# Kernel optimization log

Hardware: AMD Instinct MI355X
Metric: run time of the kernel (lower is better)

## Reference

```python
import jax, jax.numpy as jnp
import numpy as np

N_NODES = 50000
N_EDGES = 800000
HID = 128
EDGE_DIM = 4
LAYERS = 4
MAX_Z = 100
NUM_GRAPHS = 512


def setup_inputs() -> dict:
    key = jax.random.key(0)
    ks = jax.random.split(key, 16)
    s = lambda k, shape, fan_in: jax.random.normal(k, shape, jnp.float32) / np.sqrt(fan_in)
    inp = {
        "z": jax.random.randint(ks[0], (N_NODES,), 0, MAX_Z + 1),
        "edge_index": jax.random.randint(ks[1], (2, N_EDGES), 0, N_NODES),
        "edge_attr": jax.random.normal(ks[2], (N_EDGES, EDGE_DIM), jnp.float32),
        "batch": jnp.sort(jax.random.randint(ks[3], (N_NODES,), 0, NUM_GRAPHS)),
        "emb": jax.random.normal(ks[4], (MAX_Z + 1, HID), jnp.float32),
        # stacked per-layer params; Linear stored as [in, out]
        "ew1": s(ks[5], (LAYERS, 2 * HID + EDGE_DIM, HID), 2 * HID + EDGE_DIM),
        "eb1": jnp.zeros((LAYERS, HID), jnp.float32),
        "ew2": s(ks[6], (LAYERS, HID, HID), HID),
        "eb2": jnp.zeros((LAYERS, HID), jnp.float32),
        "nw": s(ks[7], (LAYERS, 2 * HID, HID), 2 * HID),
        "nb": jnp.zeros((LAYERS, HID), jnp.float32),
        "rw1": s(ks[8], (HID, HID), HID),
        "rb1": jnp.zeros((HID,), jnp.float32),
        "rw2": s(ks[9], (HID, 1), HID),
        "rb2": jnp.zeros((1,), jnp.float32),
    }
    return inp


def _forward(z, edge_index, edge_attr, batch,
             emb, ew1, eb1, ew2, eb2, nw, nb, rw1, rb1, rw2, rb2):
    silu = jax.nn.silu
    src, dst = edge_index[0], edge_index[1]
    x = emb[z]  # [N, H]
    for l in range(LAYERS):
        m_in = jnp.concatenate([x[src], x[dst], edge_attr], axis=-1)  # [E, 2H+ed]
        h = silu(m_in @ ew1[l] + eb1[l])
        msg = silu(h @ ew2[l] + eb2[l])  # [E, H]
        agg = jax.ops.segment_sum(msg, dst, num_segments=N_NODES)  # scatter-add
        x = silu(jnp.concatenate([x, agg], axis=-1) @ nw[l] + nb[l])
    # segment mean over graphs
    sums = jax.ops.segment_sum(x, batch, num_segments=NUM_GRAPHS)
    counts = jnp.clip(jax.ops.segment_sum(jnp.ones((x.shape[0],), x.dtype), batch,
                                          num_segments=NUM_GRAPHS), 1.0)[:, None]
    g = sums / counts  # [G, H]
    pred = (silu(g @ rw1 + rb1) @ rw2 + rb2)[:, 0]  # [G]
    return pred


def reference(z, edge_index, edge_attr, batch,
              emb, ew1, eb1, ew2, eb2, nw, nb, rw1, rb1, rw2, rb2):
    return _forward(z, edge_index, edge_attr, batch,
                    emb, ew1, eb1, ew2, eb2, nw, nb, rw1, rb1, rw2, rb2)
```

## Files before the change

kernel.cpp:

```cpp
#include <hip/hip_runtime.h>
#include <math.h>

#define HID  128
#define EDIM 4

typedef unsigned short u16;
typedef u16    us8   __attribute__((ext_vector_type(8)));
typedef __bf16 bf16x8 __attribute__((ext_vector_type(8)));
typedef float  f32x4 __attribute__((ext_vector_type(4)));

__device__ __forceinline__ float silu_f(float v) {
    return v * __builtin_amdgcn_rcpf(1.0f + __expf(-v));
}
__device__ __forceinline__ u16 f2bf(float f) {
    unsigned u = __float_as_uint(f);
    unsigned r = u + 0x7fffu + ((u >> 16) & 1u);
    return (u16)(r >> 16);
}
__device__ __forceinline__ u16 f2bf_fast(float f) {
    return (u16)((__float_as_uint(f) + 0x8000u) >> 16);
}
__device__ __forceinline__ unsigned pack_bf2(float a, float b) {
    return ((__float_as_uint(a) + 0x8000u) >> 16) |
           ((__float_as_uint(b) + 0x8000u) & 0xffff0000u);
}
__device__ __forceinline__ float bf2f(u16 s) {
    return __uint_as_float(((unsigned)s) << 16);
}
__device__ __forceinline__ bf16x8 as_bf(us8 v) {
    return __builtin_bit_cast(bf16x8, v);
}

__device__ __forceinline__ void wfrag_gen(const float* __restrict__ w,
        u16* __restrict__ out, int KT, int Kdata, int Kstride,
        int split, int jump, int idx) {
    int lane = idx & 63;
    int f    = (idx >> 6) % (KT * 8);
    int l    = idx / (64 * KT * 8);
    int kt = f >> 3, nt = f & 7;
    int n  = nt * 16 + (lane & 15);
    int k0 = kt * 32 + ((lane >> 4) * 8);
    us8 v;
    #pragma unroll
    for (int j = 0; j < 8; ++j) {
        int k = k0 + j;
        int row = k + (k >= split ? jump : 0);
        v[j] = (row < Kdata) ? f2bf(w[((size_t)l * Kstride + row) * HID + n]) : (u16)0;
    }
    *(us8*)&out[((size_t)(l * KT * 8 + f) * 64 + lane) * 8] = v;
}

#define T1S (4 * 4 * 8 * 64)
#define T1T (4 * 1 * 8 * 64)
#define T1B (4 * 4 * 8 * 64)
#define T2  (4 * 4 * 8 * 64)
#define T3  (4 * 8 * 8 * 64)

__global__ __launch_bounds__(256) void setup_kernel(
        const float* __restrict__ ew1, const float* __restrict__ ew2,
        const float* __restrict__ nw,
        u16* __restrict__ w1sf, u16* __restrict__ w1tf,
        u16* __restrict__ w1bf,
        u16* __restrict__ w2f, u16* __restrict__ nwf,
        int* __restrict__ cnt, int* __restrict__ cursor,
        float* __restrict__ sums, float* __restrict__ cnts_g, int N, int G) {
    const int BIG = 1 << 30;
    int idx = blockIdx.x * 256 + threadIdx.x;
    if (idx < T1S) { wfrag_gen(ew1, w1sf, 4, 128, 260, BIG, 0, idx); return; }
    idx -= T1S;
    if (idx < T1T) { wfrag_gen(ew1, w1tf, 1, 260, 260, 0, 256, idx); return; }
    idx -= T1T;
    if (idx < T1B) { wfrag_gen(ew1, w1bf, 4, 260, 260, 0, 128, idx); return; }
    idx -= T1B;
    if (idx < T2) { wfrag_gen(ew2, w2f, 4, 128, 128, BIG, 0, idx); return; }
    idx -= T2;
    if (idx < T3) { wfrag_gen(nw, nwf, 8, 256, 256, BIG, 0, idx); return; }
    idx -= T3;
    if (idx < N) { cnt[idx] = 0; return; }
    idx -= N;
    if (idx < N) { cursor[idx] = 0; return; }
    idx -= N;
    if (idx < G * HID) { sums[idx] = 0.f; return; }
    idx -= G * HID;
    if (idx < G) { cnts_g[idx] = 0.f; return; }
}

__global__ __launch_bounds__(256) void hist_kernel(const int* __restrict__ dst,
        int* __restrict__ cnt, int E) {
    int e = blockIdx.x * 256 + threadIdx.x;
    if (e < E) atomicAdd(&cnt[dst[e]], 1);
}

__global__ __launch_bounds__(1024) void scan_kernel(const int* __restrict__ cnt,
        int* __restrict__ rowptr, int n) {
    __shared__ int s[1024];
    const int t = threadIdx.x;
    const int chunk = (n + 1023) >> 10;
    int lo = t * chunk, hi = lo + chunk;
    if (lo > n) lo = n;
    if (hi > n) hi = n;
    int sum = 0;
    for (int i = lo; i < hi; ++i) sum += cnt[i];
    s[t] = sum;
    __syncthreads();
    for (int off = 1; off < 1024; off <<= 1) {
        int v = (t >= off) ? s[t - off] : 0;
        __syncthreads();
        s[t] += v;
        __syncthreads();
    }
    int run = s[t] - sum;
    for (int i = lo; i < hi; ++i) { rowptr[i] = run; run += cnt[i]; }
    if (t == 1023) rowptr[n] = run;
}

__global__ __launch_bounds__(256) void scatter_kernel(const int* __restrict__ src,
        const int* __restrict__ dst, const float* __restrict__ ea,
        const int* __restrict__ rowptr, int* __restrict__ cursor,
        int* __restrict__ srcS, int* __restrict__ dstS, u16* __restrict__ eaS, int E) {
    int e = blockIdx.x * 256 + threadIdx.x;
    if (e >= E) return;
    int d = dst[e];
    int p = rowptr[d] + atomicAdd(&cursor[d], 1);
    srcS[p] = src[e];
    dstS[p] = d;
    const float* q = &ea[(size_t)e * EDIM];
    ushort4 v;
    v.x = f2bf(q[0]); v.y = f2bf(q[1]); v.z = f2bf(q[2]); v.w = f2bf(q[3]);
    *(ushort4*)&eaS[(size_t)p * 4] = v;
}

__global__ __launch_bounds__(HID) void embed_kernel(const int* __restrict__ z,
        const float* __restrict__ emb, u16* __restrict__ xb,
        float* __restrict__ agg, const int* __restrict__ batch,
        float* __restrict__ counts, int n) {
    int i = blockIdx.x;
    if (i >= n) return;
    int t = threadIdx.x;
    xb[(size_t)i * HID + t] = f2bf(emb[(size_t)z[i] * HID + t]);
    agg[(size_t)i * HID + t] = 0.f;
    if (t == 0) unsafeAtomicAdd(&counts[batch[i]], 1.0f);
}

__global__ __launch_bounds__(256) void ys_kernel(
        const u16* __restrict__ xb, const u16* __restrict__ w1sf,
        const u16* __restrict__ w1bf,
        float* __restrict__ Ys, float* __restrict__ Y, int n) {
    const int t    = threadIdx.x;
    const int i0   = blockIdx.x * 32;
    const int wv   = t >> 6, lane = t & 63;
    const int lrow = lane & 15;
    const int kq   = lane >> 4;
    const int kq8  = kq * 8;

    int iN[2];
    #pragma unroll
    for (int mt = 0; mt < 2; ++mt) {
        int i = i0 + mt * 16 + lrow; if (i >= n) i = n - 1;
        iN[mt] = i;
    }
    f32x4 aS[2][2], aB[2][2];
    #pragma unroll
    for (int mt = 0; mt < 2; ++mt)
        #pragma unroll
        for (int nt = 0; nt < 2; ++nt) {
            aS[mt][nt] = (f32x4){0.f, 0.f, 0.f, 0.f};
            aB[mt][nt] = (f32x4){0.f, 0.f, 0.f, 0.f};
        }

    #pragma unroll
    for (int kt = 0; kt < 4; ++kt) {
        bf16x8 ws0 = *(const bf16x8*)&w1sf[((size_t)(kt * 8 + wv * 2 + 0) * 64 + lane) * 8];
        bf16x8 ws1 = *(const bf16x8*)&w1sf[((size_t)(kt * 8 + wv * 2 + 1) * 64 + lane) * 8];
        bf16x8 wb0 = *(const bf16x8*)&w1bf[((size_t)(kt * 8 + wv * 2 + 0) * 64 + lane) * 8];
        bf16x8 wb1 = *(const bf16x8*)&w1bf[((size_t)(kt * 8 + wv * 2 + 1) * 64 + lane) * 8];
        #pragma unroll
        for (int mt = 0; mt < 2; ++mt) {
            bf16x8 a = as_bf(*(const us8*)&xb[(size_t)iN[mt] * HID + kt * 32 + kq8]);
            aS[mt][0] = __builtin_amdgcn_mfma_f32_16x16x32_bf16(ws0, a, aS[mt][0], 0, 0, 0);
            aS[mt][1] = __builtin_amdgcn_mfma_f32_16x16x32_bf16(ws1, a, aS[mt][1], 0, 0, 0);
            aB[mt][0] = __builtin_amdgcn_mfma_f32_16x16x32_bf16(wb0, a, aB[mt][0], 0, 0, 0);
            aB[mt][1] = __builtin_amdgcn_mfma_f32_16x16x32_bf16(wb1, a, aB[mt][1], 0, 0, 0);
        }
    }
    #pragma unroll
    for (int mt = 0; mt < 2; ++mt) {
        int node = i0 + mt * 16 + lrow;
        if (node < n) {
            #pragma unroll
            for (int nt = 0; nt < 2; ++nt) {
                *(f32x4*)&Ys[(size_t)node * HID + (wv * 2 + nt) * 16 + kq * 4] = aS[mt][nt];
                *(f32x4*)&Y [(size_t)node * HID + (wv * 2 + nt) * 16 + kq * 4] = aB[mt][nt];
            }
        }
    }
}

__global__ __launch_bounds__(512, 8) void edge_mfma(
        const int* __restrict__ srcS, const int* __restrict__ dstS,
        const u16* __restrict__ eaS,
        const u16* __restrict__ w1tf, const float* __restrict__ b1,
        const u16* __restrict__ w2f, const float* __restrict__ b2,
        const float* __restrict__ Ys, const float* __restrict__ Y,
        float* __restrict__ agg, int nE) {
    __shared__ __align__(16) char smem[64 * 132 * 4];
    __shared__ __align__(16) int dsh[64];
    __shared__ __align__(16) int ssh[64];
    u16*   A = (u16*)smem;
    u16*   H = (u16*)smem;
    float* M = (float*)smem;

    const int t    = threadIdx.x;
    const int e0   = blockIdx.x * 64;
    const int wv   = t >> 6, lane = t & 63;
    const int lrow = lane & 15;
    const int kq   = lane >> 4;
    const int kq8  = kq * 8;
    const int rq   = kq * 4;
    const int h    = wv >> 2;
    const int p    = wv & 3;

    if (t < 64) {
        int e = e0 + t;
        bool valid = e < nE; if (!valid) e = nE - 1;
        dsh[t] = valid ? dstS[e] : -1;
        ssh[t] = srcS[e];
        ushort4 q = *(const ushort4*)&eaS[(size_t)e * 4];
        int base = t * 40;
        us8 z8 = (us8){0, 0, 0, 0, 0, 0, 0, 0};
        *(us8*)&A[base + 8]  = z8;
        *(us8*)&A[base + 16] = z8;
        *(us8*)&A[base + 24] = z8;
        A[base + 0] = q.x; A[base + 1] = q.y; A[base + 2] = q.z; A[base + 3] = q.w;
        A[base + 4] = 0;   A[base + 5] = 0;   A[base + 6] = 0;   A[base + 7] = 0;
    }
    __syncthreads();

    f32x4 acc[2][2];
    #pragma unroll
    for (int mt = 0; mt < 2; ++mt) {
        int edge = (h * 2 + mt) * 16 + lrow;
        int d = dsh[edge]; if (d < 0) d = 0;
        int s = ssh[edge];
        #pragma unroll
        for (int nt = 0; nt < 2; ++nt) {
            f32x4 bv = *(const f32x4*)&b1[(p * 2 + nt) * 16 + rq];
            f32x4 yv = *(const f32x4*)&Y [(size_t)d * HID + (p * 2 + nt) * 16 + rq];
            f32x4 sv = *(const f32x4*)&Ys[(size_t)s * HID + (p * 2 + nt) * 16 + rq];
            acc[mt][nt] = bv + yv + sv;
        }
    }
    {
        bf16x8 w0 = *(const bf16x8*)&w1tf[((size_t)(p * 2 + 0) * 64 + lane) * 8];
        bf16x8 w1 = *(const bf16x8*)&w1tf[((size_t)(p * 2 + 1) * 64 + lane) * 8];
        #pragma unroll
        for (int mt = 0; mt < 2; ++mt) {
            bf16x8 a = *(const bf16x8*)&A[((h * 2 + mt) * 16 + lrow) * 40 + kq8];
            acc[mt][0] = __builtin_amdgcn_mfma_f32_16x16x32_bf16(w0, a, acc[mt][0], 0, 0, 0);
            acc[mt][1] = __builtin_amdgcn_mfma_f32_16x16x32_bf16(w1, a, acc[mt][1], 0, 0, 0);
        }
    }
    __syncthreads();

    #pragma unroll
    for (int mt = 0; mt < 2; ++mt)
        #pragma unroll
        for (int nt = 0; nt < 2; ++nt) {
            uint2 hv;
            hv.x = pack_bf2(silu_f(acc[mt][nt][0]), silu_f(acc[mt][nt][1]));
            hv.y = pack_bf2(silu_f(acc[mt][nt][2]), silu_f(acc[mt][nt][3]));
            int edge = (h * 2 + mt) * 16 + lrow;
            *(uint2*)&H[edge * 136 + (p * 2 + nt) * 16 + rq] = hv;
        }
    __syncthreads();

    f32x4 acc2[2][2];
    #pragma unroll
    for (int nt = 0; nt < 2; ++nt) {
        f32x4 bv = *(const f32x4*)&b2[(p * 2 + nt) * 16 + rq];
        acc2[0][nt] = bv; acc2[1][nt] = bv;
    }
    #pragma unroll
    for (int kt = 0; kt < 4; ++kt) {
        bf16x8 w0 = *(const bf16x8*)&w2f[((size_t)(kt * 8 + p * 2 + 0) * 64 + lane) * 8];
        bf16x8 w1 = *(const bf16x8*)&w2f[((size_t)(kt * 8 + p * 2 + 1) * 64 + lane) * 8];
        #pragma unroll
        for (int mt = 0; mt < 2; ++mt) {
            bf16x8 a = *(const bf16x8*)&H[((h * 2 + mt) * 16 + lrow) * 136 + kt * 32 + kq8];
            acc2[mt][0] = __builtin_amdgcn_mfma_f32_16x16x32_bf16(w0, a, acc2[mt][0], 0, 0, 0);
            acc2[mt][1] = __builtin_amdgcn_mfma_f32_16x16x32_bf16(w1, a, acc2[mt][1], 0, 0, 0);
        }
    }
    __syncthreads();

    #pragma unroll
    for (int mt = 0; mt < 2; ++mt)
        #pragma unroll
        for (int nt = 0; nt < 2; ++nt) {
            f32x4 mv;
            #pragma unroll
            for (int r = 0; r < 4; ++r) mv[r] = silu_f(acc2[mt][nt][r]);
            int edge = (h * 2 + mt) * 16 + lrow;
            *(f32x4*)&M[edge * 132 + (p * 2 + nt) * 16 + rq] = mv;
        }

    {
        int col = p * 32 + (lane & 31);
        int r0  = h * 32 + (lane >> 5) * 16;
        int4 da = *(const int4*)&dsh[r0];
        int4 db = *(const int4*)&dsh[r0 + 4];
        int4 dc = *(const int4*)&dsh[r0 + 8];
        int4 dd = *(const int4*)&dsh[r0 + 12];
        int ds_[16] = {da.x, da.y, da.z, da.w, db.x, db.y, db.z, db.w,
                       dc.x, dc.y, dc.z, dc.w, dd.x, dd.y, dd.z, dd.w};
        float run = 0.f;
        int   cur = ds_[0];
        #pragma unroll
        for (int i = 0; i < 16; ++i) {
            run += M[(r0 + i) * 132 + col];
            int nxt = (i == 15) ? -2 : ds_[i + 1];
            if (cur != nxt) {
                if (cur >= 0)
                    unsafeAtomicAdd(&agg[(size_t)cur * HID + col], run);
                run = 0.f; cur = nxt;
            }
        }
    }
}

__global__ __launch_bounds__(256) void node_mfma(
        u16* __restrict__ xb, float* __restrict__ agg,
        const u16* __restrict__ nwf, const float* __restrict__ nb,
        const int* __restrict__ batch, float* __restrict__ sums,
        int last, int n) {
    const int t    = threadIdx.x;
    const int i0   = blockIdx.x * 32;
    const int wv   = t >> 6, lane = t & 63;
    const int lrow = lane & 15;
    const int kq   = lane >> 4;
    const int kq8  = kq * 8;
    const int rq   = kq * 4;

    int iN[2];
    #pragma unroll
    for (int mt = 0; mt < 2; ++mt) {
        int i = i0 + mt * 16 + lrow; if (i >= n) i = n - 1;
        iN[mt] = i;
    }

    f32x4 acc[2][2];
    {
        float bias0 = nb[wv * 32 + lrow], bias1 = nb[wv * 32 + 16 + lrow];
        #pragma unroll
        for (int mt = 0; mt < 2; ++mt)
            #pragma unroll
            for (int r = 0; r < 4; ++r) {
                acc[mt][0][r] = bias0; acc[mt][1][r] = bias1;
            }
    }
    #pragma unroll
    for (int kt = 0; kt < 4; ++kt) {
        bf16x8 w0 = *(const bf16x8*)&nwf[((size_t)(kt * 8 + wv * 2 + 0) * 64 + lane) * 8];
        bf16x8 w1 = *(const bf16x8*)&nwf[((size_t)(kt * 8 + wv * 2 + 1) * 64 + lane) * 8];
        #pragma unroll
        for (int mt = 0; mt < 2; ++mt) {
            bf16x8 a = as_bf(*(const us8*)&xb[(size_t)iN[mt] * HID + kt * 32 + kq8]);
            acc[mt][0] = __builtin_amdgcn_mfma_f32_16x16x32_bf16(a, w0, acc[mt][0], 0, 0, 0);
            acc[mt][1] = __builtin_amdgcn_mfma_f32_16x16x32_bf16(a, w1, acc[mt][1], 0, 0, 0);
        }
    }
    #pragma unroll
    for (int kt = 4; kt < 8; ++kt) {
        bf16x8 w0 = *(const bf16x8*)&nwf[((size_t)(kt * 8 + wv * 2 + 0) * 64 + lane) * 8];
        bf16x8 w1 = *(const bf16x8*)&nwf[((size_t)(kt * 8 + wv * 2 + 1) * 64 + lane) * 8];
        #pragma unroll
        for (int mt = 0; mt < 2; ++mt) {
            const float* pa = &agg[(size_t)iN[mt] * HID + (kt - 4) * 32 + kq8];
            float4 f0 = *(const float4*)pa;
            float4 f1 = *(const float4*)(pa + 4);
            us8 av;
            av[0] = f2bf_fast(f0.x); av[1] = f2bf_fast(f0.y);
            av[2] = f2bf_fast(f0.z); av[3] = f2bf_fast(f0.w);
            av[4] = f2bf_fast(f1.x); av[5] = f2bf_fast(f1.y);
            av[6] = f2bf_fast(f1.z); av[7] = f2bf_fast(f1.w);
            bf16x8 a = as_bf(av);
            acc[mt][0] = __builtin_amdgcn_mfma_f32_16x16x32_bf16(a, w0, acc[mt][0], 0, 0, 0);
            acc[mt][1] = __builtin_amdgcn_mfma_f32_16x16x32_bf16(a, w1, acc[mt][1], 0, 0, 0);
        }
    }

    if (!last) {
        __syncthreads();
        const float4 z4 = make_float4(0.f, 0.f, 0.f, 0.f);
        #pragma unroll
        for (int kt = 0; kt < 4; ++kt)
            #pragma unroll
            for (int mt = 0; mt < 2; ++mt) {
                float* pa = &agg[(size_t)iN[mt] * HID + kt * 32 + kq8];
                *(float4*)pa = z4; *(float4*)(pa + 4) = z4;
            }
        #pragma unroll
        for (int mt = 0; mt < 2; ++mt)
            #pragma unroll
            for (int nt2 = 0; nt2 < 2; ++nt2)
                #pragma unroll
                for (int r = 0; r < 4; ++r) {
                    int i = i0 + mt * 16 + rq + r;
                    if (i < n)
                        xb[(size_t)i * HID + wv * 32 + nt2 * 16 + lrow] =
                            f2bf_fast(silu_f(acc[mt][nt2][r]));
                }
    } else {
        #pragma unroll
        for (int mt = 0; mt < 2; ++mt)
            #pragma unroll
            for (int nt2 = 0; nt2 < 2; ++nt2)
                #pragma unroll
                for (int r = 0; r < 4; ++r) {
                    int i = i0 + mt * 16 + rq + r;
                    if (i < n) {
                        int b = batch[i];
                        unsafeAtomicAdd(&sums[(size_t)b * HID + wv * 32 + nt2 * 16 + lrow],
                                        silu_f(acc[mt][nt2][r]));
                    }
                }
    }
}

__global__ __launch_bounds__(HID) void readout_kernel(
        const float* __restrict__ sums, const float* __restrict__ counts,
        const float* __restrict__ rw1, const float* __restrict__ rb1,
        const float* __restrict__ rw2, const float* __restrict__ rb2,
        float* __restrict__ pred) {
    __shared__ float gv[HID];
    __shared__ float hv[HID];
    const int g = blockIdx.x;
    const int t = threadIdx.x;
    float c = counts[g];
    if (c < 1.0f) c = 1.0f;
    gv[t] = sums[(size_t)g * HID + t] / c;
    __syncthreads();
    float acc = rb1[t];
    for (int k4 = 0; k4 < 32; ++k4) {
        float4 mv = *(const float4*)&gv[k4 * 4];
        #pragma unroll
        for (int j = 0; j < 4; ++j)
            acc += ((const float*)&mv)[j] * rw1[(size_t)(k4 * 4 + j) * HID + t];
    }
    hv[t] = silu_f(acc) * rw2[t];
    __syncthreads();
    for (int s = HID / 2; s > 0; s >>= 1) {
        if (t < s) hv[t] += hv[t + s];
        __syncthreads();
    }
    if (t == 0) pred[g] = hv[0] + rb2[0];
}

extern "C" void kernel_launch(void* const* d_in, const int* in_sizes, int n_in,
                              void* d_out, int out_size, void* d_ws, size_t ws_size,
                              hipStream_t stream) {
    const int*   z          = (const int*)d_in[0];
    const int*   edge_index = (const int*)d_in[1];
    const float* edge_attr  = (const float*)d_in[2];
    const int*   batch      = (const int*)d_in[3];
    const float* emb        = (const float*)d_in[4];
    const float* ew1        = (const float*)d_in[5];
    const float* eb1        = (const float*)d_in[6];
    const float* ew2        = (const float*)d_in[7];
    const float* eb2        = (const float*)d_in[8];
    const float* nw         = (const float*)d_in[9];
    const float* nb         = (const float*)d_in[10];
    const float* rw1        = (const float*)d_in[11];
    const float* rb1        = (const float*)d_in[12];
    const float* rw2        = (const float*)d_in[13];
    const float* rb2        = (const float*)d_in[14];
    float* pred = (float*)d_out;

    const int N = in_sizes[0];
    const int E = in_sizes[1] / 2;
    const int G = out_size;
    const int* srcI = edge_index;
    const int* dstI = edge_index + E;

    char* base = (char*)d_ws;
    size_t off = 0;
    auto carve = [&](size_t bytes) -> char* {
        char* p = base + off;
        off = (off + bytes + 255) & ~(size_t)255;
        return p;
    };
    float* agg    = (float*)carve((size_t)N * HID * sizeof(float));
    float* sums   = (float*)carve((size_t)G * HID * sizeof(float));
    float* cnts_g = (float*)carve((size_t)G * sizeof(float));
    u16*   xb     = (u16*)carve((size_t)N * HID * sizeof(u16));
    float* Y      = (float*)carve((size_t)N * HID * sizeof(float));
    float* Ys     = (float*)carve((size_t)N * HID * sizeof(float));
    int*   srcS   = (int*)carve((size_t)(E + 64) * sizeof(int));
    int*   dstS   = (int*)carve((size_t)(E + 64) * sizeof(int));
    u16*   eaS    = (u16*)carve((size_t)(E + 64) * 4 * sizeof(u16));
    int*   rowptr = (int*)carve((size_t)(N + 1) * sizeof(int));
    int*   cursor = (int*)carve((size_t)N * sizeof(int));
    int*   cnt    = (int*)carve((size_t)N * sizeof(int));
    u16*   w1sf   = (u16*)carve((size_t)4 * 32 * 512 * sizeof(u16));
    u16*   w1tf   = (u16*)carve((size_t)4 * 8 * 512 * sizeof(u16));
    u16*   w1bf   = (u16*)carve((size_t)4 * 32 * 512 * sizeof(u16));
    u16*   w2f    = (u16*)carve((size_t)4 * 32 * 512 * sizeof(u16));
    u16*   nwf    = (u16*)carve((size_t)4 * 64 * 512 * sizeof(u16));

    {
        long long total = (long long)T1S + T1T + T1B + T2 + T3
                        + 2LL * N + (long long)G * HID + G;
        int blocks = (int)((total + 255) / 256);
        setup_kernel<<<blocks, 256, 0, stream>>>(ew1, ew2, nw, w1sf, w1tf, w1bf,
                                                 w2f, nwf, cnt, cursor,
                                                 sums, cnts_g, N, G);
    }

    hist_kernel<<<(E + 255) / 256, 256, 0, stream>>>(dstI, cnt, E);
    scan_kernel<<<1, 1024, 0, stream>>>(cnt, rowptr, N);
    scatter_kernel<<<(E + 255) / 256, 256, 0, stream>>>(
        srcI, dstI, edge_attr, rowptr, cursor, srcS, dstS, eaS, E);

    embed_kernel<<<N, HID, 0, stream>>>(z, emb, xb, agg, batch, cnts_g, N);

    for (int l = 0; l < 4; ++l) {
        ys_kernel<<<(N + 31) / 32, 256, 0, stream>>>(
            xb, w1sf + (size_t)l * 32 * 512, w1bf + (size_t)l * 32 * 512,
            Ys, Y, N);
        edge_mfma<<<(E + 63) / 64, 512, 0, stream>>>(
            srcS, dstS, eaS,
            w1tf + (size_t)l * 8 * 512, eb1 + (size_t)l * HID,
            w2f + (size_t)l * 32 * 512, eb2 + (size_t)l * HID,
            Ys, Y, agg, E);
        node_mfma<<<(N + 31) / 32, 256, 0, stream>>>(
            xb, agg, nwf + (size_t)l * 64 * 512, nb + (size_t)l * HID,
            batch, sums, (l == 3) ? 1 : 0, N);
    }

    readout_kernel<<<G, HID, 0, stream>>>(sums, cnts_g, rw1, rb1, rw2, rb2, pred);
}
```

Before: 1.124 ms.

## Fuse per-node dual projection into embed and node-update kernels

Removes the standalone ys_kernel by computing the next layer's source/destination projections (Ys, Y) inside the node-update kernel right after it writes the new node features, and inside a combined embed kernel for the first layer. Each block reuses its own 32 freshly written rows after a block barrier, so the x rows are read while likely still in cache and three kernel launches are saved. In exchange the node kernel becomes heavier and relies on each block reading only the rows it wrote itself.

```diff
diff --git a/kernel.cpp b/kernel.cpp
--- a/kernel.cpp
+++ b/kernel.cpp
@@ -130,24 +130,11 @@
     *(ushort4*)&eaS[(size_t)p * 4] = v;
 }
 
-__global__ __launch_bounds__(HID) void embed_kernel(const int* __restrict__ z,
-        const float* __restrict__ emb, u16* __restrict__ xb,
-        float* __restrict__ agg, const int* __restrict__ batch,
-        float* __restrict__ counts, int n) {
-    int i = blockIdx.x;
-    if (i >= n) return;
-    int t = threadIdx.x;
-    xb[(size_t)i * HID + t] = f2bf(emb[(size_t)z[i] * HID + t]);
-    agg[(size_t)i * HID + t] = 0.f;
-    if (t == 0) unsafeAtomicAdd(&counts[batch[i]], 1.0f);
-}
-
-__global__ __launch_bounds__(256) void ys_kernel(
-        const u16* __restrict__ xb, const u16* __restrict__ w1sf,
-        const u16* __restrict__ w1bf,
-        float* __restrict__ Ys, float* __restrict__ Y, int n) {
-    const int t    = threadIdx.x;
-    const int i0   = blockIdx.x * 32;
+__device__ __forceinline__ void dual_proj(
+        const u16* __restrict__ xb,
+        const u16* __restrict__ w1sf, const u16* __restrict__ w1bf,
+        float* __restrict__ Ys, float* __restrict__ Y,
+        int i0, int n, int t) {
     const int wv   = t >> 6, lane = t & 63;
     const int lrow = lane & 15;
     const int kq   = lane >> 4;
@@ -194,6 +181,29 @@
             }
         }
     }
+}
+
+__global__ __launch_bounds__(256) void embed_ys_kernel(
+        const int* __restrict__ z, const float* __restrict__ emb,
+        u16* __restrict__ xb, float* __restrict__ agg,
+        const int* __restrict__ batch, float* __restrict__ counts,
+        const u16* __restrict__ w1sf, const u16* __restrict__ w1bf,
+        float* __restrict__ Ys, float* __restrict__ Y, int n) {
+    const int t  = threadIdx.x;
+    const int i0 = blockIdx.x * 32;
+    #pragma unroll
+    for (int j = 0; j < 16; ++j) {
+        int idx = j * 256 + t;
+        int node = i0 + (idx >> 7), col = idx & 127;
+        if (node < n) {
+            xb[(size_t)node * HID + col] = f2bf(emb[(size_t)z[node] * HID + col]);
+            agg[(size_t)node * HID + col] = 0.f;
+        }
+    }
+    if (t < 32 && i0 + t < n)
+        unsafeAtomicAdd(&counts[batch[i0 + t]], 1.0f);
+    __syncthreads();
+    dual_proj(xb, w1sf, w1bf, Ys, Y, i0, n, t);
 }
 
 __global__ __launch_bounds__(512, 8) void edge_mfma(
@@ -332,6 +342,8 @@
         u16* __restrict__ xb, float* __restrict__ agg,
         const u16* __restrict__ nwf, const float* __restrict__ nb,
         const int* __restrict__ batch, float* __restrict__ sums,
+        const u16* __restrict__ w1sf_nxt, const u16* __restrict__ w1bf_nxt,
+        float* __restrict__ Ys, float* __restrict__ Y,
         int last, int n) {
     const int t    = threadIdx.x;
     const int i0   = blockIdx.x * 32;
@@ -410,6 +422,8 @@
                         xb[(size_t)i * HID + wv * 32 + nt2 * 16 + lrow] =
                             f2bf_fast(silu_f(acc[mt][nt2][r]));
                 }
+        __syncthreads();
+        dual_proj(xb, w1sf_nxt, w1bf_nxt, Ys, Y, i0, n, t);
     } else {
         #pragma unroll
         for (int mt = 0; mt < 2; ++mt)
@@ -521,20 +535,21 @@
     scatter_kernel<<<(E + 255) / 256, 256, 0, stream>>>(
         srcI, dstI, edge_attr, rowptr, cursor, srcS, dstS, eaS, E);
 
-    embed_kernel<<<N, HID, 0, stream>>>(z, emb, xb, agg, batch, cnts_g, N);
+    embed_ys_kernel<<<(N + 31) / 32, 256, 0, stream>>>(
+        z, emb, xb, agg, batch, cnts_g, w1sf, w1bf, Ys, Y, N);
 
     for (int l = 0; l < 4; ++l) {
-        ys_kernel<<<(N + 31) / 32, 256, 0, stream>>>(
-            xb, w1sf + (size_t)l * 32 * 512, w1bf + (size_t)l * 32 * 512,
-            Ys, Y, N);
         edge_mfma<<<(E + 63) / 64, 512, 0, stream>>>(
             srcS, dstS, eaS,
             w1tf + (size_t)l * 8 * 512, eb1 + (size_t)l * HID,
             w2f + (size_t)l * 32 * 512, eb2 + (size_t)l * HID,
             Ys, Y, agg, E);
+        int lnxt = (l + 1) & 3;
         node_mfma<<<(N + 31) / 32, 256, 0, stream>>>(
             xb, agg, nwf + (size_t)l * 64 * 512, nb + (size_t)l * HID,
-            batch, sums, (l == 3) ? 1 : 0, N);
+            batch, sums,
+            w1sf + (size_t)lnxt * 32 * 512, w1bf + (size_t)lnxt * 32 * 512,
+            Ys, Y, (l == 3) ? 1 : 0, N);
     }
 
     readout_kernel<<<G, HID, 0, stream>>>(sums, cnts_g, rw1, rb1, rw2, rb2, pred);
```

Result: faster. 1.075 ms (-4.4%).
